# Optimization experiments

Hardware: AMD Instinct MI355X
Metric: run time of the kernel (lower is better)

## Reference

```python
import jax, jax.numpy as jnp
import numpy as np

B, S, H = 2, 1024, 2048
NH, NKV, D = 16, 4, 128
E, K, F = 16, 2, 1408          # routed experts, top_k, moe_intermediate
FS = 1408                      # shared-expert intermediate (n_shared_experts=1)
EPS = 1e-5
RSF = 1.0                      # routed_scaling_factor


def rmsnorm(x, w):
    v = jnp.mean(jnp.square(x.astype(jnp.float32)), axis=-1, keepdims=True)
    return (x * jax.lax.rsqrt(v + EPS)).astype(x.dtype) * w


def rotate_half(x):
    x1, x2 = jnp.split(x, 2, axis=-1)
    return jnp.concatenate([-x2, x1], axis=-1)


def apply_rope(x, cos, sin):
    # x: [B,S,h,D]; cos/sin: [S,D]
    c = cos[None, :, None, :]
    s = sin[None, :, None, :]
    return x * c + rotate_half(x) * s


def setup_inputs() -> dict:
    key = jax.random.key(0)
    ks = jax.random.split(key, 16)
    sc = 0.02
    hidden_states = jax.random.normal(ks[0], (B, S, H), dtype=jnp.float32)
    # rotary embedding tables
    inv_freq = 1.0 / (10000.0 ** (np.arange(0, D, 2, dtype=np.float32) / D))
    ang = np.arange(S, dtype=np.float32)[:, None] * inv_freq[None, :]
    emb = np.concatenate([ang, ang], axis=-1)
    cos = jnp.asarray(np.cos(emb), dtype=jnp.float32)
    sin = jnp.asarray(np.sin(emb), dtype=jnp.float32)
    return {
        'hidden_states': hidden_states,
        'cos': cos,
        'sin': sin,
        'ln1_w': jnp.ones((H,), jnp.float32),
        'ln2_w': jnp.ones((H,), jnp.float32),
        'q_norm_w': jnp.ones((D,), jnp.float32),
        'k_norm_w': jnp.ones((D,), jnp.float32),
        'wq': jax.random.normal(ks[1], (H, NH * D), jnp.float32) * sc,
        'wk': jax.random.normal(ks[2], (H, NKV * D), jnp.float32) * sc,
        'wv': jax.random.normal(ks[3], (H, NKV * D), jnp.float32) * sc,
        'wo': jax.random.normal(ks[4], (NH * D, H), jnp.float32) * sc,
        'gate_w': jax.random.normal(ks[5], (E, H), jnp.float32) * sc,
        'expert_gate_up': jax.random.normal(ks[6], (E, H, 2 * F), jnp.float32) * sc,
        'expert_down': jax.random.normal(ks[7], (E, F, H), jnp.float32) * sc,
        'shared_gate_up': jax.random.normal(ks[8], (H, 2 * FS), jnp.float32) * sc,
        'shared_down': jax.random.normal(ks[9], (FS, H), jnp.float32) * sc,
    }


def silu_and_mul(gu):
    g, u = jnp.split(gu, 2, axis=-1)
    return jax.nn.silu(g) * u


def moe_block(tokens, gate_w, expert_gate_up, expert_down, shared_gate_up, shared_down):
    # tokens: [T,H]
    T = tokens.shape[0]
    router_logits = tokens.astype(jnp.float32) @ gate_w.T          # [T,E]
    probs = jax.nn.softmax(router_logits, axis=-1)
    topk_w, topk_ids = jax.lax.top_k(probs, K)                     # [T,K]
    topk_w = topk_w / jnp.sum(topk_w, axis=-1, keepdims=True)      # renormalize
    # dense combine-weight matrix [T,E] (top_k sparse routing)
    cw = jnp.zeros((T, E), jnp.float32).at[jnp.arange(T)[:, None], topk_ids].add(topk_w)
    # scan over experts: each expert is a full SwiGLU MLP on all tokens, masked by cw
    def body(acc, we):
        gw, dw, cwe = we                                            # [H,2F],[F,H],[T]
        y = silu_and_mul(tokens @ gw) @ dw                          # [T,H]
        return acc + cwe[:, None].astype(y.dtype) * y, None
    out, _ = jax.lax.scan(body, jnp.zeros_like(tokens), (expert_gate_up, expert_down, cw.T))
    out = out * RSF
    shared = silu_and_mul(tokens @ shared_gate_up) @ shared_down
    return out + shared


def reference(hidden_states, cos, sin, ln1_w, ln2_w, q_norm_w, k_norm_w,
              wq, wk, wv, wo, gate_w, expert_gate_up, expert_down,
              shared_gate_up, shared_down):
    # input layernorm (residual=None branch)
    residual = hidden_states
    x = rmsnorm(hidden_states, ln1_w)
    # attention
    q = (x @ wq).reshape(B, S, NH, D)
    k = (x @ wk).reshape(B, S, NKV, D)
    v = (x @ wv).reshape(B, S, NKV, D)
    q = rmsnorm(q, q_norm_w)
    k = rmsnorm(k, k_norm_w)
    q = apply_rope(q, cos, sin)
    k = apply_rope(k, cos, sin)
    rep = NH // NKV
    k = jnp.repeat(k, rep, axis=2)
    v = jnp.repeat(v, rep, axis=2)
    scores = jnp.einsum('bihd,bjhd->bhij', q, k) / jnp.sqrt(jnp.float32(D))
    causal = jnp.tril(jnp.ones((S, S), bool))
    scores = jnp.where(causal[None, None], scores, -jnp.inf)
    attn = jax.nn.softmax(scores, axis=-1)
    o = jnp.einsum('bhij,bjhd->bihd', attn, v).reshape(B, S, NH * D)
    attn_out = o @ wo
    # post-attention layernorm with fused residual add
    residual = residual + attn_out
    x = rmsnorm(residual, ln2_w)
    # MoE + shared expert
    tokens = x.reshape(-1, H)
    out = moe_block(tokens, gate_w, expert_gate_up, expert_down, shared_gate_up, shared_down)
    hidden = out.reshape(B, S, H)
    return hidden, residual
```

## Files before the change

### kernel.cpp

```cpp
#include <hip/hip_runtime.h>
#include <stdint.h>

typedef unsigned short u16;
typedef unsigned int   u32;
typedef __attribute__((ext_vector_type(4))) float     f32x4;
typedef __attribute__((ext_vector_type(8))) _Float16  f16x8;

#define S_LEN 1024
#define NB    2
#define H_DIM 2048
#define T_TOK 2048
#define NHEAD 16
#define NKVH  4
#define DHEAD 128
#define NEXP  16
#define FFE   1408
#define FF2   2816
#define EPSF  1e-5f
#define RSF_C 1.0f

__device__ __forceinline__ u16 f2h(float f){
  _Float16 h = (_Float16)f;
  return __builtin_bit_cast(unsigned short, h);
}
__device__ __forceinline__ void split2(float f, u16& hi, u16& lo){
  _Float16 h = (_Float16)f;
  hi = __builtin_bit_cast(unsigned short, h);
  _Float16 l = (_Float16)((f - (float)h) * 2048.0f);
  lo = __builtin_bit_cast(unsigned short, l);
}
__device__ __forceinline__ void gload_lds16(const void* g, void* l){
  __builtin_amdgcn_global_load_lds((const __attribute__((address_space(1))) void*)g,
                                   (__attribute__((address_space(3))) void*)l, 16, 0, 0);
}
__device__ __forceinline__ uint4 pack8(const u16* p){
  return make_uint4((u32)p[0] | ((u32)p[1]<<16), (u32)p[2] | ((u32)p[3]<<16),
                    (u32)p[4] | ((u32)p[5]<<16), (u32)p[6] | ((u32)p[7]<<16));
}

__global__ __launch_bounds__(256) void tsplit_all_kernel(
    const float* __restrict__ wq, const float* __restrict__ wk,
    const float* __restrict__ wv, const float* __restrict__ wo,
    const float* __restrict__ sgu, const float* __restrict__ sdn,
    u16* __restrict__ wqkvh, u16* __restrict__ wqkvl,
    u16* __restrict__ woh,  u16* __restrict__ wol,
    u16* __restrict__ sgut, u16* __restrict__ sdnt)
{
  const int z = blockIdx.z;
  const float* in; int ldn; u16* outh; u16* outl; int ldk, nx, ny; bool dual;
  switch (z) {
    case 0:  in=wq;  ldn=2048; outh=wqkvh;              outl=wqkvl;              ldk=2048; nx=32; ny=32; dual=true;  break;
    case 1:  in=wk;  ldn=512;  outh=wqkvh+2048*2048;    outl=wqkvl+2048*2048;    ldk=2048; nx=8;  ny=32; dual=true;  break;
    case 2:  in=wv;  ldn=512;  outh=wqkvh+2560*2048;    outl=wqkvl+2560*2048;    ldk=2048; nx=8;  ny=32; dual=true;  break;
    case 3:  in=wo;  ldn=2048; outh=woh;                outl=wol;                ldk=2048; nx=32; ny=32; dual=true;  break;
    case 4:  in=sgu; ldn=2816; outh=sgut;               outl=nullptr;            ldk=2048; nx=44; ny=32; dual=false; break;
    default: in=sdn; ldn=2048; outh=sdnt;               outl=nullptr;            ldk=1408; nx=32; ny=22; dual=false; break;
  }
  if ((int)blockIdx.x >= nx || (int)blockIdx.y >= ny) return;
  __shared__ float tile[64][65];
  const int n0 = blockIdx.x * 64, k0 = blockIdx.y * 64;
  const int tid = threadIdx.x;
  const int tr = tid >> 4, tc = (tid & 15) * 4;
  #pragma unroll
  for (int i = 0; i < 4; i++) {
    float4 v = *(const float4*)&in[(size_t)(k0 + tr + i*16) * ldn + (n0 + tc)];
    tile[tr + i*16][tc+0] = v.x; tile[tr + i*16][tc+1] = v.y;
    tile[tr + i*16][tc+2] = v.z; tile[tr + i*16][tc+3] = v.w;
  }
  __syncthreads();
  const int n = tid >> 2, kg = (tid & 3) * 16;
  u16 hb[16], lb[16];
  #pragma unroll
  for (int j = 0; j < 16; j++) {
    float f = tile[kg + j][n];
    if (dual) split2(f, hb[j], lb[j]); else hb[j] = f2h(f);
  }
  u16* dh = &outh[(size_t)(n0 + n) * ldk + k0 + kg];
  *(uint4*)dh       = pack8(hb);
  *(uint4*)(dh + 8) = pack8(hb + 8);
  if (dual) {
    u16* dl = &outl[(size_t)(n0 + n) * ldk + k0 + kg];
    *(uint4*)dl       = pack8(lb);
    *(uint4*)(dl + 8) = pack8(lb + 8);
  }
}

__global__ __launch_bounds__(256) void rmsnorm_kernel(
    const float* __restrict__ in, const float* __restrict__ w,
    u16* __restrict__ outh, u16* __restrict__ outl)
{
  __shared__ float red[4];
  const int t = blockIdx.x, tid = threadIdx.x;
  const int lane = tid & 63, wave = tid >> 6;
  const float* x = in + (size_t)t * H_DIM;
  const int c = tid * 8;
  float4 v0 = *(const float4*)&x[c];
  float4 v1 = *(const float4*)&x[c + 4];
  float ss = v0.x*v0.x + v0.y*v0.y + v0.z*v0.z + v0.w*v0.w
           + v1.x*v1.x + v1.y*v1.y + v1.z*v1.z + v1.w*v1.w;
  #pragma unroll
  for (int d = 1; d < 64; d <<= 1) ss += __shfl_xor(ss, d, 64);
  if (lane == 0) red[wave] = ss;
  __syncthreads();
  float rinv = rsqrtf((red[0]+red[1]+red[2]+red[3]) * (1.0f/H_DIM) + EPSF);
  float4 w0 = *(const float4*)&w[c];
  float4 w1 = *(const float4*)&w[c + 4];
  float vals[8] = { v0.x*rinv*w0.x, v0.y*rinv*w0.y, v0.z*rinv*w0.z, v0.w*rinv*w0.w,
                    v1.x*rinv*w1.x, v1.y*rinv*w1.y, v1.z*rinv*w1.z, v1.w*rinv*w1.w };
  u16 hb[8], lb[8];
  #pragma unroll
  for (int j = 0; j < 8; j++) split2(vals[j], hb[j], lb[j]);
  *(uint4*)&outh[(size_t)t * H_DIM + c] = pack8(hb);
  if (outl) *(uint4*)&outl[(size_t)t * H_DIM + c] = pack8(lb);
}

__global__ __launch_bounds__(256) void gemm3b_kernel(
    const u16* __restrict__ Ah, const u16* __restrict__ Al, int lda,
    const u16* __restrict__ Bh, const u16* __restrict__ Bl, int ldb,
    float* __restrict__ C, int ldc,
    const float* __restrict__ addsrc, int K)
{
  __shared__ u16 Ash[128*64], Asl[128*64];
  __shared__ u16 Bsh[128*64], Bsl[128*64];
  const int tid = threadIdx.x, lane = tid & 63, wave = tid >> 6;
  const int m0 = blockIdx.y * 128, n0 = blockIdx.x * 128;
  const int wm = (wave >> 1) * 64, wn = (wave & 1) * 64;
  const int arow = lane >> 3;
  const int acol = ((lane & 7) ^ arow) * 8;
  f32x4 acc0[4][4] = {}, acc1[4][4] = {};
  for (int k0 = 0; k0 < K; k0 += 64) {
    #pragma unroll
    for (int g = 0; g < 4; g++) {
      const int rb = wave*32 + g*8;
      gload_lds16(Ah + (size_t)(m0 + rb + arow)*lda + k0 + acol, &Ash[rb*64]);
      gload_lds16(Al + (size_t)(m0 + rb + arow)*lda + k0 + acol, &Asl[rb*64]);
      gload_lds16(Bh + (size_t)(n0 + rb + arow)*ldb + k0 + acol, &Bsh[rb*64]);
      gload_lds16(Bl + (size_t)(n0 + rb + arow)*ldb + k0 + acol, &Bsl[rb*64]);
    }
    asm volatile("s_waitcnt vmcnt(0) lgkmcnt(0)" ::: "memory");
    __syncthreads();
    const int fr = lane & 15, fg = lane >> 4;
    #pragma unroll
    for (int kk = 0; kk < 2; kk++) {
      const int cb = fg + kk*4;
      f16x8 ah[4], al[4];
      #pragma unroll
      for (int m = 0; m < 4; m++) {
        const int r = wm + m*16 + fr;
        const int s = (cb ^ (r & 7)) * 8;
        ah[m] = *(const f16x8*)&Ash[r*64 + s];
        al[m] = *(const f16x8*)&Asl[r*64 + s];
      }
      #pragma unroll
      for (int n = 0; n < 4; n++) {
        const int r = wn + n*16 + fr;
        const int s = (cb ^ (r & 7)) * 8;
        f16x8 bh_ = *(const f16x8*)&Bsh[r*64 + s];
        f16x8 bl_ = *(const f16x8*)&Bsl[r*64 + s];
        #pragma unroll
        for (int m = 0; m < 4; m++) {
          acc0[m][n] = __builtin_amdgcn_mfma_f32_16x16x32_f16(ah[m], bh_, acc0[m][n], 0,0,0);
          acc1[m][n] = __builtin_amdgcn_mfma_f32_16x16x32_f16(ah[m], bl_, acc1[m][n], 0,0,0);
          acc1[m][n] = __builtin_amdgcn_mfma_f32_16x16x32_f16(al[m], bh_, acc1[m][n], 0,0,0);
        }
      }
    }
    __syncthreads();
  }
  const int cr = (lane >> 4) * 4, cc = lane & 15;
  #pragma unroll
  for (int m = 0; m < 4; m++)
    #pragma unroll
    for (int n = 0; n < 4; n++)
      #pragma unroll
      for (int j = 0; j < 4; j++) {
        int r = m0 + wm + m*16 + cr + j;
        size_t idx = (size_t)r * ldc + (n0 + wn + n*16 + cc);
        float v = acc0[m][n][j] + acc1[m][n][j] * (1.0f/2048.0f);
        if (addsrc) v += addsrc[idx];
        C[idx] = v;
      }
}

__global__ __launch_bounds__(256) void gemm_up_all_kernel(
    const u16* __restrict__ Aexp, const float* __restrict__ egu, float* __restrict__ gu_exp,
    const int* __restrict__ counts, const int* __restrict__ offs,
    const int* __restrict__ tile_e, const int* __restrict__ tile_m0,
    const u16* __restrict__ tok, const u16* __restrict__ sgut, float* __restrict__ gu_sh)
{
  __shared__ u16 As[256*64];
  __shared__ u16 Bs[64*64];
  const int z = blockIdx.z;
  const int tid = threadIdx.x, lane = tid & 63, wave = tid >> 6;
  const int n0 = blockIdx.x * 64;
  const int wm = wave * 64;
  const int arow = lane >> 3;
  const int acol = ((lane & 7) ^ arow) * 8;
  const int fr = lane & 15, fg = lane >> 4;
  const int cr = (lane >> 4) * 4, cc = lane & 15;

  if (z < 32) {
    const int e = tile_e[z];
    if (e < 0) return;
    const int m0 = tile_m0[z];
    const int cnt = counts[e];
    const int off = offs[e];
    const u16* A = Aexp + (size_t)off * H_DIM;
    const float* B = egu + (size_t)e * H_DIM * FF2;
    float* C = gu_exp + (size_t)off * FF2;
    const int bn  = tid & 63;
    const int bkb = tid >> 6;
    const int bs0 = bn*64 + (((bkb*2)     ^ (bn & 7)) * 8);
    const int bs1 = bn*64 + (((bkb*2 + 1) ^ (bn & 7)) * 8);
    f32x4 acc[4][4] = {};
    for (int k0 = 0; k0 < H_DIM; k0 += 64) {
      #pragma unroll
      for (int g = 0; g < 8; g++)
        gload_lds16(A + (size_t)(m0 + wm + g*8 + arow)*H_DIM + k0 + acol,
                    &As[(wm + g*8)*64]);
      {
        const float* gb = B + (size_t)(k0 + bkb*16) * FF2 + (n0 + bn);
        float f[16];
        #pragma unroll
        for (int j = 0; j < 16; j++) f[j] = gb[(size_t)j * FF2];
        u32 pk[8];
        #pragma unroll
        for (int j = 0; j < 8; j++)
          pk[j] = __builtin_bit_cast(u32, __builtin_amdgcn_cvt_pkrtz(f[2*j], f[2*j+1]));
        *(uint4*)&Bs[bs0] = make_uint4(pk[0], pk[1], pk[2], pk[3]);
        *(uint4*)&Bs[bs1] = make_uint4(pk[4], pk[5], pk[6], pk[7]);
      }
      asm volatile("s_waitcnt vmcnt(0) lgkmcnt(0)" ::: "memory");
      __syncthreads();
      #pragma unroll
      for (int kk = 0; kk < 2; kk++) {
        const int cb = fg + kk*4;
        f16x8 a[4], b[4];
        #pragma unroll
        for (int m = 0; m < 4; m++) {
          const int r = wm + m*16 + fr;
          a[m] = *(const f16x8*)&As[r*64 + ((cb ^ (r & 7)) * 8)];
        }
        #pragma unroll
        for (int n = 0; n < 4; n++) {
          const int r = n*16 + fr;
          b[n] = *(const f16x8*)&Bs[r*64 + ((cb ^ (r & 7)) * 8)];
        }
        #pragma unroll
        for (int n = 0; n < 4; n++)
          #pragma unroll
          for (int m = 0; m < 4; m++)
            acc[m][n] = __builtin_amdgcn_mfma_f32_16x16x32_f16(a[m], b[n], acc[m][n], 0,0,0);
      }
      __syncthreads();
    }
    #pragma unroll
    for (int m = 0; m < 4; m++)
      #pragma unroll
      for (int n = 0; n < 4; n++)
        #pragma unroll
        for (int j = 0; j < 4; j++) {
          int r = m0 + wm + m*16 + cr + j;
          if (r < cnt) C[(size_t)r * FF2 + (n0 + n*16 + cc)] = acc[m][n][j];
        }
  } else {
    const int m0 = (z - 32) * 256;
    f32x4 acc[4][4] = {};
    for (int k0 = 0; k0 < H_DIM; k0 += 64) {
      #pragma unroll
      for (int g = 0; g < 8; g++)
        gload_lds16(tok + (size_t)(m0 + wm + g*8 + arow)*H_DIM + k0 + acol,
                    &As[(wm + g*8)*64]);
      #pragma unroll
      for (int g = 0; g < 2; g++)
        gload_lds16(sgut + (size_t)(n0 + wave*16 + g*8 + arow)*H_DIM + k0 + acol,
                    &Bs[(wave*16 + g*8)*64]);
      asm volatile("s_waitcnt vmcnt(0) lgkmcnt(0)" ::: "memory");
      __syncthreads();
      #pragma unroll
      for (int kk = 0; kk < 2; kk++) {
        const int cb = fg + kk*4;
        f16x8 a[4], b[4];
        #pragma unroll
        for (int m = 0; m < 4; m++) {
          const int r = wm + m*16 + fr;
          a[m] = *(const f16x8*)&As[r*64 + ((cb ^ (r & 7)) * 8)];
        }
        #pragma unroll
        for (int n = 0; n < 4; n++) {
          const int r = n*16 + fr;
          b[n] = *(const f16x8*)&Bs[r*64 + ((cb ^ (r & 7)) * 8)];
        }
        #pragma unroll
        for (int n = 0; n < 4; n++)
          #pragma unroll
          for (int m = 0; m < 4; m++)
            acc[m][n] = __builtin_amdgcn_mfma_f32_16x16x32_f16(a[m], b[n], acc[m][n], 0,0,0);
      }
      __syncthreads();
    }
    #pragma unroll
    for (int m = 0; m < 4; m++)
      #pragma unroll
      for (int n = 0; n < 4; n++)
        #pragma unroll
        for (int j = 0; j < 4; j++)
          gu_sh[(size_t)(m0 + wm + m*16 + cr + j) * FF2 + (n0 + n*16 + cc)] = acc[m][n][j];
  }
}

__global__ __launch_bounds__(256) void gemm_dn_all_kernel(
    const u16* __restrict__ Aexp, const float* __restrict__ edn, float* __restrict__ y_exp,
    const int* __restrict__ counts, const int* __restrict__ offs,
    const int* __restrict__ tile_e, const int* __restrict__ tile_m0,
    const u16* __restrict__ act_sh, const u16* __restrict__ sdnt, float* __restrict__ out_sh)
{
  __shared__ u16 As[256*64];
  __shared__ u16 Bs[64*64];
  const int z = blockIdx.z;
  const int tid = threadIdx.x, lane = tid & 63, wave = tid >> 6;
  const int n0 = blockIdx.x * 64;
  const int wm = wave * 64;
  const int arow = lane >> 3;
  const int acol = ((lane & 7) ^ arow) * 8;
  const int fr = lane & 15, fg = lane >> 4;
  const int cr = (lane >> 4) * 4, cc = lane & 15;

  if (z < 32) {
    const int e = tile_e[z];
    if (e < 0) return;
    const int m0 = tile_m0[z];
    const int cnt = counts[e];
    const int off = offs[e];
    const u16* A = Aexp + (size_t)off * FFE;
    const float* B = edn + (size_t)e * FFE * H_DIM;
    float* C = y_exp + (size_t)off * H_DIM;
    const int bn  = tid & 63;
    const int bkb = tid >> 6;
    const int bs0 = bn*64 + (((bkb*2)     ^ (bn & 7)) * 8);
    const int bs1 = bn*64 + (((bkb*2 + 1) ^ (bn & 7)) * 8);
    f32x4 acc[4][4] = {};
    for (int k0 = 0; k0 < FFE; k0 += 64) {
      #pragma unroll
      for (int g = 0; g < 8; g++)
        gload_lds16(A + (size_t)(m0 + wm + g*8 + arow)*FFE + k0 + acol,
                    &As[(wm + g*8)*64]);
      {
        const float* gb = B + (size_t)(k0 + bkb*16) * H_DIM + (n0 + bn);
        float f[16];
        #pragma unroll
        for (int j = 0; j < 16; j++) f[j] = gb[(size_t)j * H_DIM];
        u32 pk[8];
        #pragma unroll
        for (int j = 0; j < 8; j++)
          pk[j] = __builtin_bit_cast(u32, __builtin_amdgcn_cvt_pkrtz(f[2*j], f[2*j+1]));
        *(uint4*)&Bs[bs0] = make_uint4(pk[0], pk[1], pk[2], pk[3]);
        *(uint4*)&Bs[bs1] = make_uint4(pk[4], pk[5], pk[6], pk[7]);
      }
      asm volatile("s_waitcnt vmcnt(0) lgkmcnt(0)" ::: "memory");
      __syncthreads();
      #pragma unroll
      for (int kk = 0; kk < 2; kk++) {
        const int cb = fg + kk*4;
        f16x8 a[4], b[4];
        #pragma unroll
        for (int m = 0; m < 4; m++) {
          const int r = wm + m*16 + fr;
          a[m] = *(const f16x8*)&As[r*64 + ((cb ^ (r & 7)) * 8)];
        }
        #pragma unroll
        for (int n = 0; n < 4; n++) {
          const int r = n*16 + fr;
          b[n] = *(const f16x8*)&Bs[r*64 + ((cb ^ (r & 7)) * 8)];
        }
        #pragma unroll
        for (int n = 0; n < 4; n++)
          #pragma unroll
          for (int m = 0; m < 4; m++)
            acc[m][n] = __builtin_amdgcn_mfma_f32_16x16x32_f16(a[m], b[n], acc[m][n], 0,0,0);
      }
      __syncthreads();
    }
    #pragma unroll
    for (int m = 0; m < 4; m++)
      #pragma unroll
      for (int n = 0; n < 4; n++)
        #pragma unroll
        for (int j = 0; j < 4; j++) {
          int r = m0 + wm + m*16 + cr + j;
          if (r < cnt) C[(size_t)r * H_DIM + (n0 + n*16 + cc)] = acc[m][n][j];
        }
  } else {
    const int m0 = (z - 32) * 256;
    f32x4 acc[4][4] = {};
    for (int k0 = 0; k0 < FFE; k0 += 64) {
      #pragma unroll
      for (int g = 0; g < 8; g++)
        gload_lds16(act_sh + (size_t)(m0 + wm + g*8 + arow)*FFE + k0 + acol,
                    &As[(wm + g*8)*64]);
      #pragma unroll
      for (int g = 0; g < 2; g++)
        gload_lds16(sdnt + (size_t)(n0 + wave*16 + g*8 + arow)*FFE + k0 + acol,
                    &Bs[(wave*16 + g*8)*64]);
      asm volatile("s_waitcnt vmcnt(0) lgkmcnt(0)" ::: "memory");
      __syncthreads();
      #pragma unroll
      for (int kk = 0; kk < 2; kk++) {
        const int cb = fg + kk*4;
        f16x8 a[4], b[4];
        #pragma unroll
        for (int m = 0; m < 4; m++) {
          const int r = wm + m*16 + fr;
          a[m] = *(const f16x8*)&As[r*64 + ((cb ^ (r & 7)) * 8)];
        }
        #pragma unroll
        for (int n = 0; n < 4; n++) {
          const int r = n*16 + fr;
          b[n] = *(const f16x8*)&Bs[r*64 + ((cb ^ (r & 7)) * 8)];
        }
        #pragma unroll
        for (int n = 0; n < 4; n++)
          #pragma unroll
          for (int m = 0; m < 4; m++)
            acc[m][n] = __builtin_amdgcn_mfma_f32_16x16x32_f16(a[m], b[n], acc[m][n], 0,0,0);
      }
      __syncthreads();
    }
    #pragma unroll
    for (int m = 0; m < 4; m++)
      #pragma unroll
      for (int n = 0; n < 4; n++)
        #pragma unroll
        for (int j = 0; j < 4; j++)
          out_sh[(size_t)(m0 + wm + m*16 + cr + j) * H_DIM + (n0 + n*16 + cc)] = acc[m][n][j];
  }
}

__global__ __launch_bounds__(256) void rope_kernel(
    const float* __restrict__ qkv,
    const float* __restrict__ cosb, const float* __restrict__ sinb,
    const float* __restrict__ qnw, const float* __restrict__ knw,
    u16* __restrict__ qrh, u16* __restrict__ qrl,
    u16* __restrict__ krh, u16* __restrict__ krl,
    u16* __restrict__ vth, u16* __restrict__ vtl)
{
  const int jid = blockIdx.x * 4 + (threadIdx.x >> 6);
  const int lane = threadIdx.x & 63;
  const int t = jid / 24, r = jid - t*24;
  const int b = t >> 10, s = t & (S_LEN - 1);
  const float* row = qkv + (size_t)t * 3072;
  if (r < NHEAD + NKVH) {
    const bool isq = (r < NHEAD);
    const int h = isq ? r : (r - NHEAD);
    const float* x = row + (isq ? h*DHEAD : (2048 + h*DHEAD));
    const float* nw = isq ? qnw : knw;
    float x0 = x[lane], x1 = x[lane + 64];
    float ss = x0*x0 + x1*x1;
    #pragma unroll
    for (int d = 1; d < 64; d <<= 1) ss += __shfl_xor(ss, d, 64);
    float rinv = rsqrtf(ss * (1.0f/DHEAD) + EPSF);
    float n0 = x0*rinv*nw[lane], n1 = x1*rinv*nw[lane + 64];
    float o0 = n0*cosb[s*DHEAD + lane]      - n1*sinb[s*DHEAD + lane];
    float o1 = n1*cosb[s*DHEAD + lane + 64] + n0*sinb[s*DHEAD + lane + 64];
    size_t base = isq ? ((size_t)(b*NHEAD + h)*S_LEN + s)*DHEAD
                      : ((size_t)(b*NKVH + h)*S_LEN + s)*DHEAD;
    u16* dh = isq ? qrh : krh;
    u16* dl = isq ? qrl : krl;
    u16 hh, ll;
    split2(o0, hh, ll); dh[base + lane]      = hh; dl[base + lane]      = ll;
    split2(o1, hh, ll); dh[base + lane + 64] = hh; dl[base + lane + 64] = ll;
  } else {
    const int h = r - NHEAD - NKVH;
    const float* x = row + 2560 + h*DHEAD;
    size_t base = (size_t)(b*NKVH + h)*DHEAD*S_LEN + s;
    u16 hh, ll;
    split2(x[lane], hh, ll);
    vth[base + (size_t)lane*S_LEN] = hh; vtl[base + (size_t)lane*S_LEN] = ll;
    split2(x[lane + 64], hh, ll);
    vth[base + (size_t)(lane + 64)*S_LEN] = hh; vtl[base + (size_t)(lane + 64)*S_LEN] = ll;
  }
}

__global__ __launch_bounds__(256) void attn_kernel(
    const u16* __restrict__ qrh, const u16* __restrict__ qrl,
    const u16* __restrict__ krh, const u16* __restrict__ krl,
    const u16* __restrict__ vth, const u16* __restrict__ vtl,
    u16* __restrict__ oh, u16* __restrict__ ol)
{
  __shared__ u16 Kh[64*128], Kl[64*128];
  __shared__ u16 Vh[128*64], Vl[128*64];
  __shared__ u16 Ph[4*16*64], Pl[4*16*64];
  const int bx = blockIdx.x, h = blockIdx.y, b = blockIdx.z;
  const int hkv = h >> 2;
  const int lane = threadIdx.x & 63, wave = threadIdx.x >> 6;
  const int fr = lane & 15, fg = lane >> 4;
  const u16* qbh = qrh + ((size_t)(b*NHEAD + h)*S_LEN)*DHEAD;
  const u16* qbl = qrl + ((size_t)(b*NHEAD + h)*S_LEN)*DHEAD;
  const u16* kbh = krh + ((size_t)(b*NKVH + hkv)*S_LEN)*DHEAD;
  const u16* kbl = krl + ((size_t)(b*NKVH + hkv)*S_LEN)*DHEAD;
  const u16* vbh = vth + ((size_t)(b*NKVH + hkv)*DHEAD)*S_LEN;
  const u16* vbl = vtl + ((size_t)(b*NKVH + hkv)*DHEAD)*S_LEN;
  const float scl = 0.08838834764831845f;

  for (int it = 0; it < 2; it++) {
    const int qt = it ? (15 - bx) : bx;
    const int q0 = qt * 64;
    f16x8 aqh[4], aql[4];
    {
      const size_t qrow = (size_t)(q0 + wave*16 + fr)*DHEAD;
      #pragma unroll
      for (int kk = 0; kk < 4; kk++) {
        aqh[kk] = *(const f16x8*)&qbh[qrow + kk*32 + fg*8];
        aql[kk] = *(const f16x8*)&qbl[qrow + kk*32 + fg*8];
      }
    }
    f32x4 o0[8] = {}, o1[8] = {};
    float mrow[4] = {-1e30f,-1e30f,-1e30f,-1e30f};
    float lrow[4] = {0.f,0.f,0.f,0.f};
    for (int jt = 0; jt <= qt; jt++) {
      const int j0 = jt * 64;
      #pragma unroll
      for (int p = 0; p < 4; p++) {
        const int ck = p*4 + wave;
        gload_lds16(kbh + (size_t)(j0 + ck*4 + (lane>>4))*DHEAD + (lane&15)*8, &Kh[ck*512]);
        gload_lds16(kbl + (size_t)(j0 + ck*4 + (lane>>4))*DHEAD + (lane&15)*8, &Kl[ck*512]);
        gload_lds16(vbh + (size_t)(ck*8 + (lane>>3))*S_LEN + j0 + (lane&7)*8, &Vh[ck*512]);
        gload_lds16(vbl + (size_t)(ck*8 + (lane>>3))*S_LEN + j0 + (lane&7)*8, &Vl[ck*512]);
      }
      __syncthreads();
      f32x4 s0[4] = {}, s1[4] = {};
      #pragma unroll
      for (int kk = 0; kk < 4; kk++) {
        const int ko = kk*32 + fg*8;
        #pragma unroll
        for (int n = 0; n < 4; n++) {
          f16x8 bh_ = *(const f16x8*)&Kh[(n*16 + fr)*128 + ko];
          f16x8 bl_ = *(const f16x8*)&Kl[(n*16 + fr)*128 + ko];
          s0[n] = __builtin_amdgcn_mfma_f32_16x16x32_f16(aqh[kk], bh_, s0[n], 0,0,0);
          s1[n] = __builtin_amdgcn_mfma_f32_16x16x32_f16(aqh[kk], bl_, s1[n], 0,0,0);
          s1[n] = __builtin_amdgcn_mfma_f32_16x16x32_f16(aql[kk], bh_, s1[n], 0,0,0);
        }
      }
      const int rb = q0 + wave*16 + fg*4;
      float pv[4][4];
      #pragma unroll
      for (int n = 0; n < 4; n++)
        #pragma unroll
        for (int j = 0; j < 4; j++) {
          float v = (s0[n][j] + s1[n][j]*(1.0f/2048.0f)) * scl;
          if (j0 + n*16 + fr > rb + j) v = -1e30f;
          pv[n][j] = v;
        }
      float alpha[4];
      #pragma unroll
      for (int j = 0; j < 4; j++) {
        float mx = fmaxf(fmaxf(pv[0][j], pv[1][j]), fmaxf(pv[2][j], pv[3][j]));
        #pragma unroll
        for (int d = 1; d < 16; d <<= 1) mx = fmaxf(mx, __shfl_xor(mx, d, 64));
        float mnew = fmaxf(mrow[j], mx);
        alpha[j] = __expf(mrow[j] - mnew);
        mrow[j] = mnew;
      }
      float rsum[4] = {0.f,0.f,0.f,0.f};
      #pragma unroll
      for (int n = 0; n < 4; n++)
        #pragma unroll
        for (int j = 0; j < 4; j++) {
          float p = __expf(pv[n][j] - mrow[j]);
          pv[n][j] = p;
          rsum[j] += p;
        }
      #pragma unroll
      for (int j = 0; j < 4; j++) {
        #pragma unroll
        for (int d = 1; d < 16; d <<= 1) rsum[j] += __shfl_xor(rsum[j], d, 64);
        lrow[j] = lrow[j]*alpha[j] + rsum[j];
      }
      #pragma unroll
      for (int n2 = 0; n2 < 8; n2++)
        #pragma unroll
        for (int j = 0; j < 4; j++) { o0[n2][j] *= alpha[j]; o1[n2][j] *= alpha[j]; }
      #pragma unroll
      for (int n = 0; n < 4; n++)
        #pragma unroll
        for (int j = 0; j < 4; j++) {
          u16 hh, ll; split2(pv[n][j], hh, ll);
          Ph[wave*1024 + (fg*4 + j)*64 + n*16 + fr] = hh;
          Pl[wave*1024 + (fg*4 + j)*64 + n*16 + fr] = ll;
        }
      __syncthreads();
      #pragma unroll
      for (int kk = 0; kk < 2; kk++) {
        const int ko = kk*32 + fg*8;
        f16x8 ah_ = *(const f16x8*)&Ph[wave*1024 + fr*64 + ko];
        f16x8 al_ = *(const f16x8*)&Pl[wave*1024 + fr*64 + ko];
        #pragma unroll
        for (int n2 = 0; n2 < 8; n2++) {
          f16x8 vh_ = *(const f16x8*)&Vh[(n2*16 + fr)*64 + ko];
          f16x8 vl_ = *(const f16x8*)&Vl[(n2*16 + fr)*64 + ko];
          o0[n2] = __builtin_amdgcn_mfma_f32_16x16x32_f16(ah_, vh_, o0[n2], 0,0,0);
          o1[n2] = __builtin_amdgcn_mfma_f32_16x16x32_f16(ah_, vl_, o1[n2], 0,0,0);
          o1[n2] = __builtin_amdgcn_mfma_f32_16x16x32_f16(al_, vh_, o1[n2], 0,0,0);
        }
      }
      __syncthreads();
    }
    float inv[4];
    #pragma unroll
    for (int j = 0; j < 4; j++) inv[j] = 1.0f / lrow[j];
    #pragma unroll
    for (int n2 = 0; n2 < 8; n2++)
      #pragma unroll
      for (int j = 0; j < 4; j++) {
        int s = q0 + wave*16 + fg*4 + j;
        size_t idx = ((size_t)(b*S_LEN + s))*H_DIM + h*DHEAD + n2*16 + fr;
        float val = (o0[n2][j] + o1[n2][j]*(1.0f/2048.0f)) * inv[j];
        u16 hh, ll; split2(val, hh, ll);
        oh[idx] = hh; ol[idx] = ll;
      }
  }
}

__global__ __launch_bounds__(64) void router_kernel(
    const float* __restrict__ resid, const float* __restrict__ ln2w,
    const float* __restrict__ gw, int* __restrict__ ids, float* __restrict__ wts,
    int* __restrict__ counts)
{
  const int t = blockIdx.x, lane = threadIdx.x;
  const float* x = resid + (size_t)t * H_DIM;
  float xv[32];
  float ss = 0.f;
  #pragma unroll
  for (int p = 0; p < 8; p++) {
    float4 v  = *(const float4*)&x[p*256 + lane*4];
    float4 lw = *(const float4*)&ln2w[p*256 + lane*4];
    ss += v.x*v.x + v.y*v.y + v.z*v.z + v.w*v.w;
    xv[p*4+0] = v.x*lw.x; xv[p*4+1] = v.y*lw.y; xv[p*4+2] = v.z*lw.z; xv[p*4+3] = v.w*lw.w;
  }
  #pragma unroll
  for (int d = 1; d < 64; d <<= 1) ss += __shfl_xor(ss, d, 64);
  const float rinv = rsqrtf(ss * (1.0f/H_DIM) + EPSF);
  float lg[NEXP];
  #pragma unroll
  for (int e = 0; e < NEXP; e++) {
    const float* g = gw + (size_t)e * H_DIM;
    float dacc = 0.f;
    #pragma unroll
    for (int p = 0; p < 8; p++) {
      float4 gv = *(const float4*)&g[p*256 + lane*4];
      dacc += xv[p*4+0]*gv.x + xv[p*4+1]*gv.y + xv[p*4+2]*gv.z + xv[p*4+3]*gv.w;
    }
    #pragma unroll
    for (int d = 1; d < 64; d <<= 1) dacc += __shfl_xor(dacc, d, 64);
    lg[e] = dacc * rinv;
  }
  if (lane == 0) {
    int i0 = 0; float b0 = lg[0];
    #pragma unroll
    for (int e = 1; e < NEXP; e++) if (lg[e] > b0) { b0 = lg[e]; i0 = e; }
    int i1 = -1; float b1 = -3e38f;
    #pragma unroll
    for (int e = 0; e < NEXP; e++) if (e != i0 && lg[e] > b1) { b1 = lg[e]; i1 = e; }
    float rr = __expf(b1 - b0);
    float w0 = 1.0f / (1.0f + rr);
    ids[t*2] = i0; ids[t*2+1] = i1;
    wts[t*2] = w0; wts[t*2+1] = rr * w0;
    atomicAdd(&counts[i0], 1);
    atomicAdd(&counts[i1], 1);
  }
}

__global__ void scan_kernel(const int* __restrict__ counts, int* __restrict__ offs,
                            int* __restrict__ cursor,
                            int* __restrict__ tile_e, int* __restrict__ tile_m0)
{
  if (threadIdx.x == 0) {
    int s = 0, nt = 0;
    for (int e = 0; e < NEXP; e++) {
      offs[e] = s; cursor[e] = 0;
      int c = counts[e];
      for (int m0 = 0; m0 < c; m0 += 256) { tile_e[nt] = e; tile_m0[nt] = m0; nt++; }
      s += c;
    }
    for (; nt < 32; nt++) { tile_e[nt] = -1; tile_m0[nt] = 0; }
  }
}

__global__ __launch_bounds__(256) void scatter_kernel(
    const int* __restrict__ ids, const int* __restrict__ offs,
    int* __restrict__ cursor, int* __restrict__ list, int* __restrict__ pos)
{
  int t = blockIdx.x * 256 + threadIdx.x;
  if (t < T_TOK) {
    for (int kk = 0; kk < 2; kk++) {
      int e = ids[t*2 + kk];
      int p = atomicAdd(&cursor[e], 1);
      int i = offs[e] + p;
      list[i] = t;
      pos[t*2 + kk] = i;
    }
  }
}

__global__ __launch_bounds__(256) void gather_kernel(
    const u16* __restrict__ tok, const int* __restrict__ list, u16* __restrict__ aexp)
{
  const int i = blockIdx.x;
  const int t = list[i];
  const int c = threadIdx.x * 8;
  *(uint4*)&aexp[(size_t)i*H_DIM + c] = *(const uint4*)&tok[(size_t)t*H_DIM + c];
}

__global__ __launch_bounds__(256) void silu_all_kernel(
    const float* __restrict__ gu_exp, u16* __restrict__ act_ex,
    const float* __restrict__ gu_sh,  u16* __restrict__ act_sh)
{
  const int rr = blockIdx.x;
  const float* g;
  u16* o;
  if (rr < 2*T_TOK) { g = gu_exp + (size_t)rr * FF2;          o = act_ex + (size_t)rr * FFE; }
  else              { g = gu_sh  + (size_t)(rr - 2*T_TOK) * FF2; o = act_sh + (size_t)(rr - 2*T_TOK) * FFE; }
  for (int c = threadIdx.x*4; c < FFE; c += 1024) {
    float4 gv = *(const float4*)&g[c];
    float4 uv = *(const float4*)&g[c + FFE];
    float s0 = gv.x / (1.0f + __expf(-gv.x)) * uv.x;
    float s1 = gv.y / (1.0f + __expf(-gv.y)) * uv.y;
    float s2 = gv.z / (1.0f + __expf(-gv.z)) * uv.z;
    float s3 = gv.w / (1.0f + __expf(-gv.w)) * uv.w;
    u32 lo = (u32)f2h(s0) | ((u32)f2h(s1) << 16);
    u32 hi = (u32)f2h(s2) | ((u32)f2h(s3) << 16);
    *(uint2*)&o[c] = make_uint2(lo, hi);
  }
}

__global__ __launch_bounds__(256) void combine_kernel(
    const float* __restrict__ y,
    const int* __restrict__ pos, const float* __restrict__ wts,
    float* __restrict__ out)
{
  const int t = blockIdx.x;
  const int p0 = pos[t*2], p1 = pos[t*2+1];
  const float w0 = wts[t*2] * RSF_C, w1 = wts[t*2+1] * RSF_C;
  const int c = threadIdx.x * 8;
  #pragma unroll
  for (int q = 0; q < 2; q++) {
    const int cc = c + q*4;
    float4 s  = *(const float4*)&out[(size_t)t*H_DIM + cc];
    float4 a  = *(const float4*)&y[(size_t)p0*H_DIM + cc];
    float4 bb = *(const float4*)&y[(size_t)p1*H_DIM + cc];
    float4 r;
    r.x = s.x + w0*a.x + w1*bb.x;
    r.y = s.y + w0*a.y + w1*bb.y;
    r.z = s.z + w0*a.z + w1*bb.z;
    r.w = s.w + w0*a.w + w1*bb.w;
    *(float4*)&out[(size_t)t*H_DIM + cc] = r;
  }
}

extern "C" void kernel_launch(void* const* d_in, const int* in_sizes, int n_in,
                              void* d_out, int out_size, void* d_ws, size_t ws_size,
                              hipStream_t stream)
{
  (void)in_sizes; (void)n_in; (void)out_size;
  const float* hidden = (const float*)d_in[0];
  const float* cosb   = (const float*)d_in[1];
  const float* sinb   = (const float*)d_in[2];
  const float* ln1w   = (const float*)d_in[3];
  const float* ln2w   = (const float*)d_in[4];
  const float* qnw    = (const float*)d_in[5];
  const float* knw    = (const float*)d_in[6];
  const float* wq     = (const float*)d_in[7];
  const float* wk     = (const float*)d_in[8];
  const float* wv     = (const float*)d_in[9];
  const float* wo     = (const float*)d_in[10];
  const float* gw     = (const float*)d_in[11];
  const float* egu    = (const float*)d_in[12];
  const float* edn    = (const float*)d_in[13];
  const float* sgu    = (const float*)d_in[14];
  const float* sdn    = (const float*)d_in[15];
  float* out_hidden = (float*)d_out;
  float* resid = (float*)d_out + (size_t)T_TOK * H_DIM;

  char* ws = (char*)d_ws;
  constexpr size_t OFF_XH    = 0;
  constexpr size_t OFF_XL    = 8388608;
  constexpr size_t OFF_WQKVH = 16777216;
  constexpr size_t OFF_WQKVL = 29360128;
  constexpr size_t OFF_WOH   = 41943040;
  constexpr size_t OFF_WOL   = 50331648;
  constexpr size_t OFF_QKV   = 58720256;
  constexpr size_t OFF_QRH = 16777216, OFF_QRL = 25165824;
  constexpr size_t OFF_KRH = 33554432, OFF_KRL = 35651584;
  constexpr size_t OFF_VTH = 37748736, OFF_VTL = 39845888;
  constexpr size_t OFF_OH = 58720256, OFF_OL = 67108864;
  constexpr size_t OFF_GUE = 0;
  constexpr size_t OFF_AEX = 46137344;
  constexpr size_t OFF_TOK = 63963136;
  constexpr size_t OFF_ACE = 72351744;
  constexpr size_t OFF_GUS = 84606976;
  constexpr size_t OFF_ACS = 107675648;
  constexpr size_t OFF_SGUT= 113442816;
  constexpr size_t OFF_SDNT= 124977152;
  constexpr size_t OFF_IDS = 130744320;
  constexpr size_t OFF_WTS = OFF_IDS + 16384;
  constexpr size_t OFF_POS = OFF_WTS + 16384;
  constexpr size_t OFF_LST = OFF_POS + 16384;
  constexpr size_t OFF_CNT = OFF_LST + 16384;
  constexpr size_t OFF_OFS = OFF_CNT + 64;
  constexpr size_t OFF_CUR = OFF_OFS + 64;
  constexpr size_t OFF_TE  = OFF_CUR + 64;
  constexpr size_t OFF_TM  = OFF_TE + 128;
  constexpr size_t WS_NEED = OFF_TM + 128;
  if (ws_size < WS_NEED) return;

  u16* xh     = (u16*)(ws + OFF_XH);
  u16* xl     = (u16*)(ws + OFF_XL);
  u16* wqkvh  = (u16*)(ws + OFF_WQKVH);
  u16* wqkvl  = (u16*)(ws + OFF_WQKVL);
  u16* woh    = (u16*)(ws + OFF_WOH);
  u16* wol    = (u16*)(ws + OFF_WOL);
  float* qkv  = (float*)(ws + OFF_QKV);
  u16* q_rh = (u16*)(ws + OFF_QRH);
  u16* q_rl = (u16*)(ws + OFF_QRL);
  u16* k_rh = (u16*)(ws + OFF_KRH);
  u16* k_rl = (u16*)(ws + OFF_KRL);
  u16* v_th = (u16*)(ws + OFF_VTH);
  u16* v_tl = (u16*)(ws + OFF_VTL);
  u16* o_h  = (u16*)(ws + OFF_OH);
  u16* o_l  = (u16*)(ws + OFF_OL);
  float* gu_exp = (float*)(ws + OFF_GUE);
  float* y_exp  = (float*)(ws + OFF_GUE);
  u16* a_exp    = (u16*)(ws + OFF_AEX);
  u16* tok      = (u16*)(ws + OFF_TOK);
  u16* act_ex   = (u16*)(ws + OFF_ACE);
  float* gu_sh  = (float*)(ws + OFF_GUS);
  u16* act_sh   = (u16*)(ws + OFF_ACS);
  u16* sgut     = (u16*)(ws + OFF_SGUT);
  u16* sdnt     = (u16*)(ws + OFF_SDNT);
  int* ids    = (int*)(ws + OFF_IDS);
  float* wts  = (float*)(ws + OFF_WTS);
  int* pos    = (int*)(ws + OFF_POS);
  int* list   = (int*)(ws + OFF_LST);
  int* counts = (int*)(ws + OFF_CNT);
  int* offs   = (int*)(ws + OFF_OFS);
  int* cursor = (int*)(ws + OFF_CUR);
  int* tile_e = (int*)(ws + OFF_TE);
  int* tile_m0= (int*)(ws + OFF_TM);

  hipMemsetAsync(counts, 0, 64, stream);

  tsplit_all_kernel<<<dim3(44,32,6), 256, 0, stream>>>(wq, wk, wv, wo, sgu, sdn,
                                                       wqkvh, wqkvl, woh, wol, sgut, sdnt);

  rmsnorm_kernel<<<T_TOK, 256, 0, stream>>>(hidden, ln1w, xh, xl);
  gemm3b_kernel<<<dim3(24,16), 256, 0, stream>>>(xh, xl, H_DIM, wqkvh, wqkvl, 2048, qkv, 3072, nullptr, H_DIM);
  rope_kernel<<<(T_TOK*24)/4, 256, 0, stream>>>(qkv, cosb, sinb, qnw, knw,
                                                q_rh, q_rl, k_rh, k_rl, v_th, v_tl);
  attn_kernel<<<dim3(8, NHEAD, NB), 256, 0, stream>>>(q_rh, q_rl, k_rh, k_rl, v_th, v_tl, o_h, o_l);
  gemm3b_kernel<<<dim3(16,16), 256, 0, stream>>>(o_h, o_l, H_DIM, woh, wol, 2048, resid, H_DIM, hidden, H_DIM);

  rmsnorm_kernel<<<T_TOK, 256, 0, stream>>>(resid, ln2w, tok, nullptr);
  router_kernel<<<T_TOK, 64, 0, stream>>>(resid, ln2w, gw, ids, wts, counts);
  scan_kernel<<<1, 64, 0, stream>>>(counts, offs, cursor, tile_e, tile_m0);
  scatter_kernel<<<8, 256, 0, stream>>>(ids, offs, cursor, list, pos);
  gather_kernel<<<2*T_TOK, 256, 0, stream>>>(tok, list, a_exp);

  gemm_up_all_kernel<<<dim3(44,1,40), 256, 0, stream>>>(a_exp, egu, gu_exp,
                                                        counts, offs, tile_e, tile_m0,
                                                        tok, sgut, gu_sh);
  silu_all_kernel<<<3*T_TOK, 256, 0, stream>>>(gu_exp, act_ex, gu_sh, act_sh);
  gemm_dn_all_kernel<<<dim3(32,1,40), 256, 0, stream>>>(act_ex, edn, y_exp,
                                                        counts, offs, tile_e, tile_m0,
                                                        act_sh, sdnt, out_hidden);
  combine_kernel<<<T_TOK, 256, 0, stream>>>(y_exp, pos, wts, out_hidden);
}
```

Baseline: 746.8 us.

## Double MoE GEMM K-tile to 128 and fuse the post-attention RMSNorm into the router

The expert and shared-expert up/down GEMMs now stage 128-wide K slices in LDS instead of 64. The LDS swizzle is widened to 16 column blocks to match. This halves the number of barrier and wait cycles per K loop, at the cost of doubling LDS per block, which may lower how many blocks fit on a CU. Separately, the router kernel now writes the normalized fp16 token rows itself, so the standalone rmsnorm launch and its extra read of the residual are removed.

```diff
diff --git a/kernel.cpp b/kernel.cpp
--- a/kernel.cpp
+++ b/kernel.cpp
@@ -188,14 +188,14 @@
     const int* __restrict__ tile_e, const int* __restrict__ tile_m0,
     const u16* __restrict__ tok, const u16* __restrict__ sgut, float* __restrict__ gu_sh)
 {
-  __shared__ u16 As[256*64];
-  __shared__ u16 Bs[64*64];
+  __shared__ u16 As[256*128];
+  __shared__ u16 Bs[64*128];
   const int z = blockIdx.z;
   const int tid = threadIdx.x, lane = tid & 63, wave = tid >> 6;
   const int n0 = blockIdx.x * 64;
   const int wm = wave * 64;
-  const int arow = lane >> 3;
-  const int acol = ((lane & 7) ^ arow) * 8;
+  const int arow4 = lane >> 4;
+  const int abase = (lane & 15) ^ arow4;
   const int fr = lane & 15, fg = lane >> 4;
   const int cr = (lane >> 4) * 4, cc = lane & 15;
 
@@ -209,43 +209,47 @@
     const float* B = egu + (size_t)e * H_DIM * FF2;
     float* C = gu_exp + (size_t)off * FF2;
     const int bn  = tid & 63;
-    const int bkb = tid >> 6;
-    const int bs0 = bn*64 + (((bkb*2)     ^ (bn & 7)) * 8);
-    const int bs1 = bn*64 + (((bkb*2 + 1) ^ (bn & 7)) * 8);
+    const int bwv = tid >> 6;
     f32x4 acc[4][4] = {};
-    for (int k0 = 0; k0 < H_DIM; k0 += 64) {
-      #pragma unroll
-      for (int g = 0; g < 8; g++)
-        gload_lds16(A + (size_t)(m0 + wm + g*8 + arow)*H_DIM + k0 + acol,
-                    &As[(wm + g*8)*64]);
+    for (int k0 = 0; k0 < H_DIM; k0 += 128) {
+      #pragma unroll
+      for (int g = 0; g < 16; g++) {
+        const int colblk = abase ^ ((g & 3) << 2);
+        gload_lds16(A + (size_t)(m0 + wm + g*4 + arow4)*H_DIM + k0 + colblk*8,
+                    &As[(wm + g*4)*128]);
+      }
       {
-        const float* gb = B + (size_t)(k0 + bkb*16) * FF2 + (n0 + bn);
-        float f[16];
-        #pragma unroll
-        for (int j = 0; j < 16; j++) f[j] = gb[(size_t)j * FF2];
-        u32 pk[8];
-        #pragma unroll
-        for (int j = 0; j < 8; j++)
-          pk[j] = __builtin_bit_cast(u32, __builtin_amdgcn_cvt_pkrtz(f[2*j], f[2*j+1]));
-        *(uint4*)&Bs[bs0] = make_uint4(pk[0], pk[1], pk[2], pk[3]);
-        *(uint4*)&Bs[bs1] = make_uint4(pk[4], pk[5], pk[6], pk[7]);
+        const float* gb = B + (size_t)(k0 + bwv*32) * FF2 + (n0 + bn);
+        #pragma unroll
+        for (int half = 0; half < 2; half++) {
+          float f[16];
+          #pragma unroll
+          for (int j = 0; j < 16; j++) f[j] = gb[(size_t)(half*16 + j) * FF2];
+          u32 pk[8];
+          #pragma unroll
+          for (int j = 0; j < 8; j++)
+            pk[j] = __builtin_bit_cast(u32, __builtin_amdgcn_cvt_pkrtz(f[2*j], f[2*j+1]));
+          #pragma unroll
+          for (int i = 0; i < 2; i++) {
+            const int cb = bwv*4 + half*2 + i;
+            *(uint4*)&Bs[bn*128 + ((cb ^ (bn & 15)) * 8)] =
+                make_uint4(pk[i*4], pk[i*4+1], pk[i*4+2], pk[i*4+3]);
+          }
+        }
       }
       asm volatile("s_waitcnt vmcnt(0) lgkmcnt(0)" ::: "memory");
       __syncthreads();
       #pragma unroll
-      for (int kk = 0; kk < 2; kk++) {
+      for (int kk = 0; kk < 4; kk++) {
         const int cb = fg + kk*4;
+        const int s = (cb ^ fr) * 8;
         f16x8 a[4], b[4];
         #pragma unroll
-        for (int m = 0; m < 4; m++) {
-          const int r = wm + m*16 + fr;
-          a[m] = *(const f16x8*)&As[r*64 + ((cb ^ (r & 7)) * 8)];
-        }
-        #pragma unroll
-        for (int n = 0; n < 4; n++) {
-          const int r = n*16 + fr;
-          b[n] = *(const f16x8*)&Bs[r*64 + ((cb ^ (r & 7)) * 8)];
-        }
+        for (int m = 0; m < 4; m++)
+          a[m] = *(const f16x8*)&As[(wm + m*16 + fr)*128 + s];
+        #pragma unroll
+        for (int n = 0; n < 4; n++)
+          b[n] = *(const f16x8*)&Bs[(n*16 + fr)*128 + s];
         #pragma unroll
         for (int n = 0; n < 4; n++)
           #pragma unroll
@@ -266,31 +270,32 @@
   } else {
     const int m0 = (z - 32) * 256;
     f32x4 acc[4][4] = {};
-    for (int k0 = 0; k0 < H_DIM; k0 += 64) {
-      #pragma unroll
-      for (int g = 0; g < 8; g++)
-        gload_lds16(tok + (size_t)(m0 + wm + g*8 + arow)*H_DIM + k0 + acol,
-                    &As[(wm + g*8)*64]);
-      #pragma unroll
-      for (int g = 0; g < 2; g++)
-        gload_lds16(sgut + (size_t)(n0 + wave*16 + g*8 + arow)*H_DIM + k0 + acol,
-                    &Bs[(wave*16 + g*8)*64]);
+    for (int k0 = 0; k0 < H_DIM; k0 += 128) {
+      #pragma unroll
+      for (int g = 0; g < 16; g++) {
+        const int colblk = abase ^ ((g & 3) << 2);
+        gload_lds16(tok + (size_t)(m0 + wm + g*4 + arow4)*H_DIM + k0 + colblk*8,
+                    &As[(wm + g*4)*128]);
+      }
+      #pragma unroll
+      for (int g = 0; g < 4; g++) {
+        const int colblk = abase ^ ((g & 3) << 2);
+        gload_lds16(sgut + (size_t)(n0 + wave*16 + g*4 + arow4)*H_DIM + k0 + colblk*8,
+                    &Bs[(wave*16 + g*4)*128]);
+      }
       asm volatile("s_waitcnt vmcnt(0) lgkmcnt(0)" ::: "memory");
       __syncthreads();
       #pragma unroll
-      for (int kk = 0; kk < 2; kk++) {
+      for (int kk = 0; kk < 4; kk++) {
         const int cb = fg + kk*4;
+        const int s = (cb ^ fr) * 8;
         f16x8 a[4], b[4];
         #pragma unroll
-        for (int m = 0; m < 4; m++) {
-          const int r = wm + m*16 + fr;
-          a[m] = *(const f16x8*)&As[r*64 + ((cb ^ (r & 7)) * 8)];
-        }
-        #pragma unroll
-        for (int n = 0; n < 4; n++) {
-          const int r = n*16 + fr;
-          b[n] = *(const f16x8*)&Bs[r*64 + ((cb ^ (r & 7)) * 8)];
-        }
+        for (int m = 0; m < 4; m++)
+          a[m] = *(const f16x8*)&As[(wm + m*16 + fr)*128 + s];
+        #pragma unroll
+        for (int n = 0; n < 4; n++)
+          b[n] = *(const f16x8*)&Bs[(n*16 + fr)*128 + s];
         #pragma unroll
         for (int n = 0; n < 4; n++)
           #pragma unroll
@@ -315,14 +320,14 @@
     const int* __restrict__ tile_e, const int* __restrict__ tile_m0,
     const u16* __restrict__ act_sh, const u16* __restrict__ sdnt, float* __restrict__ out_sh)
 {
-  __shared__ u16 As[256*64];
-  __shared__ u16 Bs[64*64];
+  __shared__ u16 As[256*128];
+  __shared__ u16 Bs[64*128];
   const int z = blockIdx.z;
   const int tid = threadIdx.x, lane = tid & 63, wave = tid >> 6;
   const int n0 = blockIdx.x * 64;
   const int wm = wave * 64;
-  const int arow = lane >> 3;
-  const int acol = ((lane & 7) ^ arow) * 8;
+  const int arow4 = lane >> 4;
+  const int abase = (lane & 15) ^ arow4;
   const int fr = lane & 15, fg = lane >> 4;
   const int cr = (lane >> 4) * 4, cc = lane & 15;
 
@@ -336,43 +341,47 @@
     const float* B = edn + (size_t)e * FFE * H_DIM;
     float* C = y_exp + (size_t)off * H_DIM;
     const int bn  = tid & 63;
-    const int bkb = tid >> 6;
-    const int bs0 = bn*64 + (((bkb*2)     ^ (bn & 7)) * 8);
-    const int bs1 = bn*64 + (((bkb*2 + 1) ^ (bn & 7)) * 8);
+    const int bwv = tid >> 6;
     f32x4 acc[4][4] = {};
-    for (int k0 = 0; k0 < FFE; k0 += 64) {
-      #pragma unroll
-      for (int g = 0; g < 8; g++)
-        gload_lds16(A + (size_t)(m0 + wm + g*8 + arow)*FFE + k0 + acol,
-                    &As[(wm + g*8)*64]);
+    for (int k0 = 0; k0 < FFE; k0 += 128) {
+      #pragma unroll
+      for (int g = 0; g < 16; g++) {
+        const int colblk = abase ^ ((g & 3) << 2);
+        gload_lds16(A + (size_t)(m0 + wm + g*4 + arow4)*FFE + k0 + colblk*8,
+                    &As[(wm + g*4)*128]);
+      }
       {
-        const float* gb = B + (size_t)(k0 + bkb*16) * H_DIM + (n0 + bn);
-        float f[16];
-        #pragma unroll
-        for (int j = 0; j < 16; j++) f[j] = gb[(size_t)j * H_DIM];
-        u32 pk[8];
-        #pragma unroll
-        for (int j = 0; j < 8; j++)
-          pk[j] = __builtin_bit_cast(u32, __builtin_amdgcn_cvt_pkrtz(f[2*j], f[2*j+1]));
-        *(uint4*)&Bs[bs0] = make_uint4(pk[0], pk[1], pk[2], pk[3]);
-        *(uint4*)&Bs[bs1] = make_uint4(pk[4], pk[5], pk[6], pk[7]);
+        const float* gb = B + (size_t)(k0 + bwv*32) * H_DIM + (n0 + bn);
+        #pragma unroll
+        for (int half = 0; half < 2; half++) {
+          float f[16];
+          #pragma unroll
+          for (int j = 0; j < 16; j++) f[j] = gb[(size_t)(half*16 + j) * H_DIM];
+          u32 pk[8];
+          #pragma unroll
+          for (int j = 0; j < 8; j++)
+            pk[j] = __builtin_bit_cast(u32, __builtin_amdgcn_cvt_pkrtz(f[2*j], f[2*j+1]));
+          #pragma unroll
+          for (int i = 0; i < 2; i++) {
+            const int cb = bwv*4 + half*2 + i;
+            *(uint4*)&Bs[bn*128 + ((cb ^ (bn & 15)) * 8)] =
+                make_uint4(pk[i*4], pk[i*4+1], pk[i*4+2], pk[i*4+3]);
+          }
+        }
       }
       asm volatile("s_waitcnt vmcnt(0) lgkmcnt(0)" ::: "memory");
       __syncthreads();
       #pragma unroll
-      for (int kk = 0; kk < 2; kk++) {
+      for (int kk = 0; kk < 4; kk++) {
         const int cb = fg + kk*4;
+        const int s = (cb ^ fr) * 8;
         f16x8 a[4], b[4];
         #pragma unroll
-        for (int m = 0; m < 4; m++) {
-          const int r = wm + m*16 + fr;
-          a[m] = *(const f16x8*)&As[r*64 + ((cb ^ (r & 7)) * 8)];
-        }
-        #pragma unroll
-        for (int n = 0; n < 4; n++) {
-          const int r = n*16 + fr;
-          b[n] = *(const f16x8*)&Bs[r*64 + ((cb ^ (r & 7)) * 8)];
-        }
+        for (int m = 0; m < 4; m++)
+          a[m] = *(const f16x8*)&As[(wm + m*16 + fr)*128 + s];
+        #pragma unroll
+        for (int n = 0; n < 4; n++)
+          b[n] = *(const f16x8*)&Bs[(n*16 + fr)*128 + s];
         #pragma unroll
         for (int n = 0; n < 4; n++)
           #pragma unroll
@@ -393,31 +402,32 @@
   } else {
     const int m0 = (z - 32) * 256;
     f32x4 acc[4][4] = {};
-    for (int k0 = 0; k0 < FFE; k0 += 64) {
-      #pragma unroll
-      for (int g = 0; g < 8; g++)
-        gload_lds16(act_sh + (size_t)(m0 + wm + g*8 + arow)*FFE + k0 + acol,
-                    &As[(wm + g*8)*64]);
-      #pragma unroll
-      for (int g = 0; g < 2; g++)
-        gload_lds16(sdnt + (size_t)(n0 + wave*16 + g*8 + arow)*FFE + k0 + acol,
-                    &Bs[(wave*16 + g*8)*64]);
+    for (int k0 = 0; k0 < FFE; k0 += 128) {
+      #pragma unroll
+      for (int g = 0; g < 16; g++) {
+        const int colblk = abase ^ ((g & 3) << 2);
+        gload_lds16(act_sh + (size_t)(m0 + wm + g*4 + arow4)*FFE + k0 + colblk*8,
+                    &As[(wm + g*4)*128]);
+      }
+      #pragma unroll
+      for (int g = 0; g < 4; g++) {
+        const int colblk = abase ^ ((g & 3) << 2);
+        gload_lds16(sdnt + (size_t)(n0 + wave*16 + g*4 + arow4)*FFE + k0 + colblk*8,
+                    &Bs[(wave*16 + g*4)*128]);
+      }
       asm volatile("s_waitcnt vmcnt(0) lgkmcnt(0)" ::: "memory");
       __syncthreads();
       #pragma unroll
-      for (int kk = 0; kk < 2; kk++) {
+      for (int kk = 0; kk < 4; kk++) {
         const int cb = fg + kk*4;
+        const int s = (cb ^ fr) * 8;
         f16x8 a[4], b[4];
         #pragma unroll
-        for (int m = 0; m < 4; m++) {
-          const int r = wm + m*16 + fr;
-          a[m] = *(const f16x8*)&As[r*64 + ((cb ^ (r & 7)) * 8)];
-        }
-        #pragma unroll
-        for (int n = 0; n < 4; n++) {
-          const int r = n*16 + fr;
-          b[n] = *(const f16x8*)&Bs[r*64 + ((cb ^ (r & 7)) * 8)];
-        }
+        for (int m = 0; m < 4; m++)
+          a[m] = *(const f16x8*)&As[(wm + m*16 + fr)*128 + s];
+        #pragma unroll
+        for (int n = 0; n < 4; n++)
+          b[n] = *(const f16x8*)&Bs[(n*16 + fr)*128 + s];
         #pragma unroll
         for (int n = 0; n < 4; n++)
           #pragma unroll
@@ -624,7 +634,7 @@
 __global__ __launch_bounds__(64) void router_kernel(
     const float* __restrict__ resid, const float* __restrict__ ln2w,
     const float* __restrict__ gw, int* __restrict__ ids, float* __restrict__ wts,
-    int* __restrict__ counts)
+    int* __restrict__ counts, u16* __restrict__ tok)
 {
   const int t = blockIdx.x, lane = threadIdx.x;
   const float* x = resid + (size_t)t * H_DIM;
@@ -640,6 +650,13 @@
   #pragma unroll
   for (int d = 1; d < 64; d <<= 1) ss += __shfl_xor(ss, d, 64);
   const float rinv = rsqrtf(ss * (1.0f/H_DIM) + EPSF);
+  u16* tokrow = tok + (size_t)t * H_DIM;
+  #pragma unroll
+  for (int p = 0; p < 8; p++) {
+    u32 lo = (u32)f2h(xv[p*4+0]*rinv) | ((u32)f2h(xv[p*4+1]*rinv) << 16);
+    u32 hi = (u32)f2h(xv[p*4+2]*rinv) | ((u32)f2h(xv[p*4+3]*rinv) << 16);
+    *(uint2*)&tokrow[p*256 + lane*4] = make_uint2(lo, hi);
+  }
   float lg[NEXP];
   #pragma unroll
   for (int e = 0; e < NEXP; e++) {
@@ -859,8 +876,7 @@
   attn_kernel<<<dim3(8, NHEAD, NB), 256, 0, stream>>>(q_rh, q_rl, k_rh, k_rl, v_th, v_tl, o_h, o_l);
   gemm3b_kernel<<<dim3(16,16), 256, 0, stream>>>(o_h, o_l, H_DIM, woh, wol, 2048, resid, H_DIM, hidden, H_DIM);
 
-  rmsnorm_kernel<<<T_TOK, 256, 0, stream>>>(resid, ln2w, tok, nullptr);
-  router_kernel<<<T_TOK, 64, 0, stream>>>(resid, ln2w, gw, ids, wts, counts);
+  router_kernel<<<T_TOK, 64, 0, stream>>>(resid, ln2w, gw, ids, wts, counts, tok);
   scan_kernel<<<1, 64, 0, stream>>>(counts, offs, cursor, tile_e, tile_m0);
   scatter_kernel<<<8, 256, 0, stream>>>(ids, offs, cursor, list, pos);
   gather_kernel<<<2*T_TOK, 256, 0, stream>>>(tok, list, a_exp);
```

After: 776.4 us. +4.0%, slower.
